# Kernel optimization log

Hardware: AMD Instinct MI355X
Metric: run time of the kernel (lower is better)

The kernel has to match this reference:

```python
import jax, jax.numpy as jnp
import numpy as np

B, T, MEL, C, NL, NSTATE, NFREQ = 16, 1024, 80, 512, 6, 32, 513

def _layer_norm(x, g, b, eps=1e-5):
    mu = x.mean(-1, keepdims=True)
    var = ((x - mu) ** 2).mean(-1, keepdims=True)
    return (x - mu) * jax.lax.rsqrt(var + eps) * g + b

def _s4d(h, logA, Cp, Dp):
    # h: [B,T,C]; diagonal S4D: K[c,t] = sum_n Cp[c,n] * exp(-exp(logA[c,n]) * t)
    t = jnp.arange(T, dtype=h.dtype)
    A = -jnp.exp(logA)                                   # [C,N]
    expA = jnp.exp(A[:, :, None] * t)                    # [C,N,T] Vandermonde
    K = jnp.einsum('cn,cnt->tc', Cp, expA)               # [T,C]
    n_fft = 2 * T
    Xf = jnp.fft.rfft(h, n=n_fft, axis=1)                # [B,F,C]
    Kf = jnp.fft.rfft(K, n=n_fft, axis=0)                # [F,C]
    y = jnp.fft.irfft(Xf * Kf[None], n=n_fft, axis=1)[:, :T, :]
    return jax.nn.gelu(y + Dp * h)

def setup_inputs() -> dict:
    key = jax.random.key(0)
    ks = jax.random.split(key, 16)
    f32 = jnp.float32
    inp = {
        'mel': jax.random.normal(ks[0], (B, T, MEL), f32),
        'w_in': jax.random.normal(ks[1], (MEL, C), f32) * (MEL ** -0.5),
        'b_in': jnp.zeros((C,), f32),
        'freq_emb': jax.random.normal(ks[2], (NFREQ, C), f32) * 0.02,
        's4_logA': jnp.log(0.5 * jnp.ones((NL, C, NSTATE), f32))
                   + 0.1 * jax.random.normal(ks[3], (NL, C, NSTATE), f32),
        's4_C': jax.random.normal(ks[4], (NL, C, NSTATE), f32) * (NSTATE ** -0.5),
        's4_D': jax.random.normal(ks[5], (NL, 1, 1, C), f32),
        'ln_g': jnp.ones((6, C), f32),
        'ln_b': jnp.zeros((6, C), f32),
        'w5': jax.random.normal(ks[6], (5, C), f32) * (C ** -0.5),
        'b5': jnp.zeros((5,), f32),
        'wm': jax.random.normal(ks[7], (C, 13), f32) * (C ** -0.5),
        'bm': jnp.zeros((13,), f32),
    }
    return inp

def reference(mel, w_in, b_in, freq_emb, s4_logA, s4_C, s4_D, ln_g, ln_b, w5, b5, wm, bm):
    x = mel @ w_in + b_in                                # [B,T,C]
    # pad/truncate freq positional embedding along time to T
    if NFREQ >= T:
        freq = freq_emb[:T]
    else:
        pad = jnp.broadcast_to(freq_emb[-1:], (T - NFREQ, C))
        freq = jnp.concatenate([freq_emb, pad], axis=0)
    h = x + freq[None]                                   # [B,T,C]
    for l in range(NL):
        h = _s4d(h, s4_logA[l], s4_C[l], s4_D[l])
    hm = h.mean(axis=1)                                  # [B,C]
    f0        = (_layer_norm(h,  ln_g[0], ln_b[0]) @ w5[0] + b5[0])        # [B,T]
    energy    = (_layer_norm(h,  ln_g[1], ln_b[1]) @ w5[1] + b5[1])        # [B,T]
    pitch_var = (_layer_norm(h,  ln_g[2], ln_b[2]) @ w5[2] + b5[2])        # [B,T]
    speech_rate = (_layer_norm(hm, ln_g[3], ln_b[3]) @ w5[3] + b5[3])[:, None]  # [B,1]
    pause_dur   = (_layer_norm(hm, ln_g[4], ln_b[4]) @ w5[4] + b5[4])[:, None]  # [B,1]
    mfcc        = _layer_norm(hm, ln_g[5], ln_b[5]) @ wm + bm              # [B,13]
    return (f0, energy, pitch_var, speech_rate, pause_dur, mfcc)
```

## Files before the change

kernel.cpp:

```cpp
#include <hip/hip_runtime.h>
#include <hip/hip_bf16.h>

#define B_ 16
#define T_ 1024
#define MEL_ 80
#define C_ 512
#define NL_ 6
#define NS_ 32
#define HBSTR 1096

typedef _Float16 f16x8 __attribute__((ext_vector_type(8)));
typedef float f32x4 __attribute__((ext_vector_type(4)));

__device__ __forceinline__ float wred(float v) {
#pragma unroll
    for (int m = 32; m >= 1; m >>= 1) v += __shfl_xor(v, m, 64);
    return v;
}

__device__ __forceinline__ unsigned int pkh(float a, float b) {
    typedef __fp16 h2 __attribute__((ext_vector_type(2)));
    h2 r = __builtin_amdgcn_cvt_pkrtz(a, b);
    return __builtin_bit_cast(unsigned int, r);
}
__device__ __forceinline__ float h2f(unsigned short u) {
    return (float)__builtin_bit_cast(_Float16, u);
}

__global__ __launch_bounds__(256) void tap_frags(const float* __restrict__ logA,
                                                 const float* __restrict__ Cp,
                                                 const float* __restrict__ Dp,
                                                 unsigned short* __restrict__ AH,
                                                 unsigned short* __restrict__ AL) {
    __shared__ float KT[4][32];
    const int gid0 = blockIdx.x * 4;
    const int tid = threadIdx.x;
    if (tid < 128) {
        int gl = tid >> 5, tau = tid & 31;
        int gid = gid0 + gl;
        const float* la = logA + (size_t)gid * NS_;
        const float* cp = Cp + (size_t)gid * NS_;
        float s = 0.f;
        float t = (float)tau;
#pragma unroll 8
        for (int n = 0; n < NS_; ++n)
            s += cp[n] * expf(-expf(la[n]) * t);
        if (tau == 0) s += Dp[gid];
        KT[gl][tau] = s;
    }
    __syncthreads();
    const int wv = tid >> 6, lane = tid & 63;
    const int gid = gid0 + wv;
    float kv = KT[wv][lane & 31];
    const int m = lane & 15, hh = lane >> 4;
    f16x8 vh, vl;
#pragma unroll
    for (int e = 0; e < 8; ++e) {
        int th = 32 + m - 8 * hh - e;
        int tl = m - 8 * hh - e;
        float a = __shfl(kv, th & 31, 64);
        float bq = __shfl(kv, tl & 31, 64);
        vh[e] = (th >= 0 && th < 32) ? (_Float16)a : (_Float16)0.f;
        vl[e] = (tl >= 0 && tl < 32) ? (_Float16)bq : (_Float16)0.f;
    }
    *(f16x8*)(AH + (size_t)gid * 512 + lane * 8) = vh;
    *(f16x8*)(AL + (size_t)gid * 512 + lane * 8) = vl;
}

__global__ __launch_bounds__(512) void conv_stack(const float* __restrict__ mel,
                                                  const float* __restrict__ w_in,
                                                  const float* __restrict__ b_in,
                                                  const float* __restrict__ freq,
                                                  const unsigned short* __restrict__ AH,
                                                  const unsigned short* __restrict__ AL,
                                                  unsigned short* __restrict__ hfin,
                                                  float* __restrict__ hm) {
    __shared__ unsigned short HB[8 * HBSTR];
    const int b = blockIdx.y;
    const int gx = blockIdx.x;
    const int c0 = 8 * (((gx & 7) << 3) | (gx >> 3));
    const int tid = threadIdx.x;
    const int lane = tid & 63;
    const int wv = tid >> 6;
    const int c = __builtin_amdgcn_readfirstlane(c0 + wv);
    unsigned short* hb = &HB[wv * HBSTR];
    const int n = lane & 15, hh = lane >> 4;

    if (lane < 32) hb[lane] = 0;
    if (lane < 40) hb[1056 + lane] = 0;

    {
        f16x8 Wf[3];
#pragma unroll
        for (int ch = 0; ch < 3; ++ch) {
            f16x8 w;
#pragma unroll
            for (int e = 0; e < 8; ++e) {
                int k = 32 * ch + 8 * hh + e;
                float v = (n < 8 && k < MEL_) ? w_in[(size_t)k * C_ + c0 + n] : 0.f;
                w[e] = (_Float16)v;
            }
            Wf[ch] = w;
        }
        float biasn = (n < 8) ? b_in[c0 + n] : 0.f;
        const float* melb = mel + (size_t)b * T_ * MEL_;
#pragma unroll
        for (int tt = 0; tt < 8; ++tt) {
            const int tbase = 128 * wv + 16 * tt;
            f16x8 Am[3];
#pragma unroll
            for (int ch = 0; ch < 3; ++ch) {
                f16x8 a = {0, 0, 0, 0, 0, 0, 0, 0};
                if (ch < 2 || hh < 2) {
                    const float* mp = melb + (size_t)(tbase + n) * MEL_ + 32 * ch + 8 * hh;
                    float4 m0 = *(const float4*)(mp);
                    float4 m1 = *(const float4*)(mp + 4);
                    a[0] = (_Float16)m0.x; a[1] = (_Float16)m0.y;
                    a[2] = (_Float16)m0.z; a[3] = (_Float16)m0.w;
                    a[4] = (_Float16)m1.x; a[5] = (_Float16)m1.y;
                    a[6] = (_Float16)m1.z; a[7] = (_Float16)m1.w;
                }
                Am[ch] = a;
            }
            f32x4 d = {0.f, 0.f, 0.f, 0.f};
            d = __builtin_amdgcn_mfma_f32_16x16x32_f16(Am[0], Wf[0], d, 0, 0, 0);
            d = __builtin_amdgcn_mfma_f32_16x16x32_f16(Am[1], Wf[1], d, 0, 0, 0);
            d = __builtin_amdgcn_mfma_f32_16x16x32_f16(Am[2], Wf[2], d, 0, 0, 0);
            if (n < 8) {
                float v[4];
#pragma unroll
                for (int r = 0; r < 4; ++r) {
                    int t = tbase + 4 * hh + r;
                    int fr = t < 513 ? t : 512;
                    v[r] = d[r] + biasn + freq[(size_t)fr * C_ + c0 + n];
                }
                uint2 pw;
                pw.x = pkh(v[0], v[1]);
                pw.y = pkh(v[2], v[3]);
                *(uint2*)(&HB[n * HBSTR + 32 + tbase + 4 * hh]) = pw;
            }
        }
    }
    __syncthreads();

    const int boff = 16 * n + 8 * hh;
    const int woff = 32 + 16 * n + 4 * hh;

    f16x8 Ah = *(const f16x8*)(AH + (size_t)c * 512 + lane * 8);
    f16x8 Al = *(const f16x8*)(AL + (size_t)c * 512 + lane * 8);

    float hsum = 0.f;
    for (int l = 0; l < NL_; ++l) {
        const int ln = (l + 1 < NL_) ? l + 1 : 0;
        f16x8 nAh = *(const f16x8*)(AH + ((size_t)ln * C_ + c) * 512 + lane * 8);
        f16x8 nAl = *(const f16x8*)(AL + ((size_t)ln * C_ + c) * 512 + lane * 8);

        f32x4 d[4];
#pragma unroll
        for (int q = 0; q < 4; ++q) {
            const unsigned short* base = hb + 256 * q + boff;
            f16x8 Bh = *(const f16x8*)(base);
            f16x8 Bl = *(const f16x8*)(base + 32);
            f32x4 z = {0.f, 0.f, 0.f, 0.f};
            d[q] = __builtin_amdgcn_mfma_f32_16x16x32_f16(Ah, Bh, z, 0, 0, 0);
            d[q] = __builtin_amdgcn_mfma_f32_16x16x32_f16(Al, Bl, d[q], 0, 0, 0);
        }
#pragma unroll
        for (int q = 0; q < 4; ++q) {
            float g[4];
#pragma unroll
            for (int r = 0; r < 4; ++r) {
                float y = d[q][r];
                float u2 = y * (y * y * 0.07135481627f + 1.59576912161f);
                float rr = __builtin_amdgcn_rcpf(__expf(u2) + 1.f);
                g[r] = y - y * rr;
            }
            if (l == NL_ - 1) hsum += g[0] + g[1] + g[2] + g[3];
            uint2 pw;
            pw.x = pkh(g[0], g[1]);
            pw.y = pkh(g[2], g[3]);
            *(uint2*)(&hb[woff + 256 * q]) = pw;
        }
        Ah = nAh; Al = nAl;
    }

    {
        float s = wred(hsum);
        if (lane == 0) hm[(size_t)b * C_ + c] = s * (1.f / T_);
    }

    __syncthreads();
    {
        unsigned short* dst = hfin + (size_t)b * T_ * C_ + c0;
#pragma unroll
        for (int it = 0; it < 4; ++it) {
            int idx = it * 512 + tid;
            int t = idx >> 1, u = idx & 1;
            unsigned int w0 = (unsigned int)HB[(4 * u + 0) * HBSTR + 32 + t] |
                              ((unsigned int)HB[(4 * u + 1) * HBSTR + 32 + t] << 16);
            unsigned int w1 = (unsigned int)HB[(4 * u + 2) * HBSTR + 32 + t] |
                              ((unsigned int)HB[(4 * u + 3) * HBSTR + 32 + t] << 16);
            uint2 pw = {w0, w1};
            *(uint2*)(dst + (size_t)t * C_ + 4 * u) = pw;
        }
    }
}

__global__ __launch_bounds__(256) void heads_rows(const unsigned short* __restrict__ h,
                                                  const float* __restrict__ ln_g,
                                                  const float* __restrict__ ln_b,
                                                  const float* __restrict__ w5,
                                                  const float* __restrict__ b5,
                                                  float* __restrict__ out) {
    int wv = threadIdx.x >> 6, lane = threadIdx.x & 63;
    int r0 = blockIdx.x * 16 + wv * 4;
    float g[3][8], bb[3][8], ww[3][8];
#pragma unroll
    for (int o = 0; o < 3; ++o) {
        const float* gp = ln_g + o * C_ + lane * 8;
        const float* bp = ln_b + o * C_ + lane * 8;
        const float* wp = w5 + o * C_ + lane * 8;
        float4 a, bq;
        a = *(const float4*)(gp); bq = *(const float4*)(gp + 4);
        g[o][0]=a.x; g[o][1]=a.y; g[o][2]=a.z; g[o][3]=a.w;
        g[o][4]=bq.x; g[o][5]=bq.y; g[o][6]=bq.z; g[o][7]=bq.w;
        a = *(const float4*)(bp); bq = *(const float4*)(bp + 4);
        bb[o][0]=a.x; bb[o][1]=a.y; bb[o][2]=a.z; bb[o][3]=a.w;
        bb[o][4]=bq.x; bb[o][5]=bq.y; bb[o][6]=bq.z; bb[o][7]=bq.w;
        a = *(const float4*)(wp); bq = *(const float4*)(wp + 4);
        ww[o][0]=a.x; ww[o][1]=a.y; ww[o][2]=a.z; ww[o][3]=a.w;
        ww[o][4]=bq.x; ww[o][5]=bq.y; ww[o][6]=bq.z; ww[o][7]=bq.w;
    }
    float b5r[3] = {b5[0], b5[1], b5[2]};
#pragma unroll
    for (int rr = 0; rr < 4; ++rr) {
        const int r = r0 + rr;
        const unsigned short* row = h + (size_t)r * C_ + lane * 8;
        float x[8];
        {
            uint4 q = *(const uint4*)(row);
            x[0] = h2f((unsigned short)(q.x & 0xffff));
            x[1] = h2f((unsigned short)(q.x >> 16));
            x[2] = h2f((unsigned short)(q.y & 0xffff));
            x[3] = h2f((unsigned short)(q.y >> 16));
            x[4] = h2f((unsigned short)(q.z & 0xffff));
            x[5] = h2f((unsigned short)(q.z >> 16));
            x[6] = h2f((unsigned short)(q.w & 0xffff));
            x[7] = h2f((unsigned short)(q.w >> 16));
        }
        float s = 0.f;
#pragma unroll
        for (int i = 0; i < 8; ++i) s += x[i];
        float mu = wred(s) * (1.f / C_);
        float v = 0.f;
#pragma unroll
        for (int i = 0; i < 8; ++i) { float d = x[i] - mu; v += d * d; }
        float rstd = rsqrtf(wred(v) * (1.f / C_) + 1e-5f);
#pragma unroll
        for (int o = 0; o < 3; ++o) {
            float acc = 0.f;
#pragma unroll
            for (int i = 0; i < 8; ++i) {
                float xn = (x[i] - mu) * rstd * g[o][i] + bb[o][i];
                acc += xn * ww[o][i];
            }
            acc = wred(acc);
            if (lane == 0) out[o * (B_ * T_) + r] = acc + b5r[o];
        }
    }
}

__global__ __launch_bounds__(64) void heads_utt(const float* __restrict__ hm,
                                                const float* __restrict__ ln_g,
                                                const float* __restrict__ ln_b,
                                                const float* __restrict__ w5,
                                                const float* __restrict__ b5,
                                                const float* __restrict__ wm,
                                                const float* __restrict__ bm,
                                                float* __restrict__ out) {
    int b = blockIdx.x;
    int lane = threadIdx.x;
    const float* row = hm + (size_t)b * C_;
    float x[8];
#pragma unroll
    for (int i = 0; i < 8; ++i) x[i] = row[lane + 64 * i];
    float s = 0.f;
#pragma unroll
    for (int i = 0; i < 8; ++i) s += x[i];
    float mu = wred(s) * (1.f / C_);
    float v = 0.f;
#pragma unroll
    for (int i = 0; i < 8; ++i) { float d = x[i] - mu; v += d * d; }
    float rstd = rsqrtf(wred(v) * (1.f / C_) + 1e-5f);

    const int OUT_SR = 3 * B_ * T_;
    const int OUT_PD = OUT_SR + B_;
    const int OUT_MF = OUT_PD + B_;
#pragma unroll
    for (int o = 3; o <= 4; ++o) {
        float acc = 0.f;
#pragma unroll
        for (int i = 0; i < 8; ++i) {
            int cc = lane + 64 * i;
            float xn = (x[i] - mu) * rstd * ln_g[o * C_ + cc] + ln_b[o * C_ + cc];
            acc += xn * w5[o * C_ + cc];
        }
        acc = wred(acc);
        if (lane == 0) out[(o == 3 ? OUT_SR : OUT_PD) + b] = acc + b5[o];
    }
    float mf[13];
#pragma unroll
    for (int j = 0; j < 13; ++j) mf[j] = 0.f;
#pragma unroll
    for (int i = 0; i < 8; ++i) {
        int cc = lane + 64 * i;
        float xn = (x[i] - mu) * rstd * ln_g[5 * C_ + cc] + ln_b[5 * C_ + cc];
#pragma unroll
        for (int j = 0; j < 13; ++j) mf[j] += xn * wm[cc * 13 + j];
    }
#pragma unroll
    for (int j = 0; j < 13; ++j) {
        float m = wred(mf[j]);
        if (lane == 0) out[OUT_MF + b * 13 + j] = m + bm[j];
    }
}

extern "C" void kernel_launch(void* const* d_in, const int* in_sizes, int n_in,
                              void* d_out, int out_size, void* d_ws, size_t ws_size,
                              hipStream_t stream) {
    const float* mel   = (const float*)d_in[0];
    const float* w_in  = (const float*)d_in[1];
    const float* b_in  = (const float*)d_in[2];
    const float* freq  = (const float*)d_in[3];
    const float* logA  = (const float*)d_in[4];
    const float* s4C   = (const float*)d_in[5];
    const float* s4D   = (const float*)d_in[6];
    const float* ln_g  = (const float*)d_in[7];
    const float* ln_b  = (const float*)d_in[8];
    const float* w5    = (const float*)d_in[9];
    const float* b5    = (const float*)d_in[10];
    const float* wm    = (const float*)d_in[11];
    const float* bm    = (const float*)d_in[12];
    float* out = (float*)d_out;

    char* ws = (char*)d_ws;
    const size_t H16 = (size_t)B_ * T_ * C_ * sizeof(unsigned short);
    unsigned short* hB16 = (unsigned short*)ws;
    float* hm = (float*)(ws + H16);
    unsigned short* AH = (unsigned short*)(ws + H16 +
                                           (size_t)B_ * C_ * sizeof(float));
    unsigned short* AL = AH + (size_t)NL_ * C_ * 512;

    tap_frags<<<(NL_ * C_) / 4, 256, 0, stream>>>(logA, s4C, s4D, AH, AL);
    conv_stack<<<dim3(C_ / 8, B_), 512, 0, stream>>>(mel, w_in, b_in, freq,
                                                     AH, AL, hB16, hm);
    heads_rows<<<(B_ * T_) / 16, 256, 0, stream>>>(hB16, ln_g, ln_b, w5, b5, out);
    heads_utt<<<B_, 64, 0, stream>>>(hm, ln_g, ln_b, w5, b5, wm, bm, out);
}
```

Measured before the change: 153.4 us.

## Split input projection into separate kernel and store activations in fp32

Moves the mel-to-channel projection and frequency embedding add out of conv_stack into a new in_proj kernel. in_proj writes a channel-major fp32 buffer, and conv_stack loads it into shared memory instead of running MFMA on mel. The final hidden state is now written and read as fp32 instead of fp16, which doubles its traffic to heads_rows. The change adds an extra kernel launch and a full-size fp32 round trip through global memory, apparently in exchange for better precision or simpler staging.

Measured after the change: 154.0 us. No clear change (+0.3%).

```diff
diff --git a/kernel.cpp b/kernel.cpp
--- a/kernel.cpp
+++ b/kernel.cpp
@@ -67,13 +67,71 @@
     *(f16x8*)(AL + (size_t)gid * 512 + lane * 8) = vl;
 }
 
-__global__ __launch_bounds__(512) void conv_stack(const float* __restrict__ mel,
-                                                  const float* __restrict__ w_in,
-                                                  const float* __restrict__ b_in,
-                                                  const float* __restrict__ freq,
+__global__ __launch_bounds__(256) void in_proj(const float* __restrict__ mel,
+                                               const float* __restrict__ w_in,
+                                               const float* __restrict__ b_in,
+                                               const float* __restrict__ freq,
+                                               float* __restrict__ h0T) {
+    const int wid = blockIdx.x * 4 + (threadIdx.x >> 6);
+    const int lane = threadIdx.x & 63;
+    const int mtile = wid >> 1;
+    const int chalf = wid & 1;
+    const int rbase = mtile * 16;
+    const int b = rbase >> 10;
+    const int tloc = rbase & 1023;
+    const int n = lane & 15, hh = lane >> 4;
+
+    f16x8 Am[3];
+#pragma unroll
+    for (int ch = 0; ch < 3; ++ch) {
+        f16x8 a = {0, 0, 0, 0, 0, 0, 0, 0};
+        if (ch < 2 || hh < 2) {
+            const float* mp = mel + (size_t)(rbase + n) * MEL_ + 32 * ch + 8 * hh;
+            float4 m0 = *(const float4*)(mp);
+            float4 m1 = *(const float4*)(mp + 4);
+            a[0] = (_Float16)m0.x; a[1] = (_Float16)m0.y;
+            a[2] = (_Float16)m0.z; a[3] = (_Float16)m0.w;
+            a[4] = (_Float16)m1.x; a[5] = (_Float16)m1.y;
+            a[6] = (_Float16)m1.z; a[7] = (_Float16)m1.w;
+        }
+        Am[ch] = a;
+    }
+
+#pragma unroll 4
+    for (int it = 0; it < 16; ++it) {
+        const int ct = chalf * 256 + it * 16;
+        const int c = ct + n;
+        f16x8 Bw[3];
+#pragma unroll
+        for (int ch = 0; ch < 3; ++ch) {
+            f16x8 w = {0, 0, 0, 0, 0, 0, 0, 0};
+            if (ch < 2 || hh < 2) {
+#pragma unroll
+                for (int e = 0; e < 8; ++e)
+                    w[e] = (_Float16)w_in[(size_t)(32 * ch + 8 * hh + e) * C_ + c];
+            }
+            Bw[ch] = w;
+        }
+        f32x4 d = {0.f, 0.f, 0.f, 0.f};
+        d = __builtin_amdgcn_mfma_f32_16x16x32_f16(Am[0], Bw[0], d, 0, 0, 0);
+        d = __builtin_amdgcn_mfma_f32_16x16x32_f16(Am[1], Bw[1], d, 0, 0, 0);
+        d = __builtin_amdgcn_mfma_f32_16x16x32_f16(Am[2], Bw[2], d, 0, 0, 0);
+        float bias = b_in[c];
+        float4 v;
+#pragma unroll
+        for (int r = 0; r < 4; ++r) {
+            int t = tloc + 4 * hh + r;
+            int fr = t < 513 ? t : 512;
+            ((float*)&v)[r] = d[r] + bias + freq[(size_t)fr * C_ + c];
+        }
+        *(float4*)(h0T + ((size_t)b * C_ + c) * T_ + tloc + 4 * hh) = v;
+    }
+}
+
+__global__ __launch_bounds__(512) void conv_stack(const float* __restrict__ h0T,
+                                                  float* __restrict__ hfin,
                                                   const unsigned short* __restrict__ AH,
                                                   const unsigned short* __restrict__ AL,
-                                                  unsigned short* __restrict__ hfin,
                                                   float* __restrict__ hm) {
     __shared__ unsigned short HB[8 * HBSTR];
     const int b = blockIdx.y;
@@ -84,65 +142,26 @@
     const int wv = tid >> 6;
     const int c = __builtin_amdgcn_readfirstlane(c0 + wv);
     unsigned short* hb = &HB[wv * HBSTR];
-    const int n = lane & 15, hh = lane >> 4;
 
     if (lane < 32) hb[lane] = 0;
     if (lane < 40) hb[1056 + lane] = 0;
 
     {
-        f16x8 Wf[3];
-#pragma unroll
-        for (int ch = 0; ch < 3; ++ch) {
-            f16x8 w;
-#pragma unroll
-            for (int e = 0; e < 8; ++e) {
-                int k = 32 * ch + 8 * hh + e;
-                float v = (n < 8 && k < MEL_) ? w_in[(size_t)k * C_ + c0 + n] : 0.f;
-                w[e] = (_Float16)v;
-            }
-            Wf[ch] = w;
-        }
-        float biasn = (n < 8) ? b_in[c0 + n] : 0.f;
-        const float* melb = mel + (size_t)b * T_ * MEL_;
-#pragma unroll
-        for (int tt = 0; tt < 8; ++tt) {
-            const int tbase = 128 * wv + 16 * tt;
-            f16x8 Am[3];
-#pragma unroll
-            for (int ch = 0; ch < 3; ++ch) {
-                f16x8 a = {0, 0, 0, 0, 0, 0, 0, 0};
-                if (ch < 2 || hh < 2) {
-                    const float* mp = melb + (size_t)(tbase + n) * MEL_ + 32 * ch + 8 * hh;
-                    float4 m0 = *(const float4*)(mp);
-                    float4 m1 = *(const float4*)(mp + 4);
-                    a[0] = (_Float16)m0.x; a[1] = (_Float16)m0.y;
-                    a[2] = (_Float16)m0.z; a[3] = (_Float16)m0.w;
-                    a[4] = (_Float16)m1.x; a[5] = (_Float16)m1.y;
-                    a[6] = (_Float16)m1.z; a[7] = (_Float16)m1.w;
-                }
-                Am[ch] = a;
-            }
-            f32x4 d = {0.f, 0.f, 0.f, 0.f};
-            d = __builtin_amdgcn_mfma_f32_16x16x32_f16(Am[0], Wf[0], d, 0, 0, 0);
-            d = __builtin_amdgcn_mfma_f32_16x16x32_f16(Am[1], Wf[1], d, 0, 0, 0);
-            d = __builtin_amdgcn_mfma_f32_16x16x32_f16(Am[2], Wf[2], d, 0, 0, 0);
-            if (n < 8) {
-                float v[4];
-#pragma unroll
-                for (int r = 0; r < 4; ++r) {
-                    int t = tbase + 4 * hh + r;
-                    int fr = t < 513 ? t : 512;
-                    v[r] = d[r] + biasn + freq[(size_t)fr * C_ + c0 + n];
-                }
-                uint2 pw;
-                pw.x = pkh(v[0], v[1]);
-                pw.y = pkh(v[2], v[3]);
-                *(uint2*)(&HB[n * HBSTR + 32 + tbase + 4 * hh]) = pw;
-            }
-        }
-    }
-    __syncthreads();
-
+        const float* srcT = h0T + ((size_t)b * C_ + c) * T_ + 16 * lane;
+        float4 e0 = *(const float4*)(srcT);
+        float4 e1 = *(const float4*)(srcT + 4);
+        float4 e2 = *(const float4*)(srcT + 8);
+        float4 e3 = *(const float4*)(srcT + 12);
+        uint4 p0, p1;
+        p0.x = pkh(e0.x, e0.y); p0.y = pkh(e0.z, e0.w);
+        p0.z = pkh(e1.x, e1.y); p0.w = pkh(e1.z, e1.w);
+        p1.x = pkh(e2.x, e2.y); p1.y = pkh(e2.z, e2.w);
+        p1.z = pkh(e3.x, e3.y); p1.w = pkh(e3.z, e3.w);
+        *(uint4*)(&hb[32 + 16 * lane]) = p0;
+        *(uint4*)(&hb[32 + 16 * lane + 8]) = p1;
+    }
+
+    const int n = lane & 15, hh = lane >> 4;
     const int boff = 16 * n + 8 * hh;
     const int woff = 32 + 16 * n + 4 * hh;
 
@@ -191,22 +210,22 @@
 
     __syncthreads();
     {
-        unsigned short* dst = hfin + (size_t)b * T_ * C_ + c0;
+        float* dst = hfin + (size_t)b * T_ * C_ + c0;
 #pragma unroll
         for (int it = 0; it < 4; ++it) {
             int idx = it * 512 + tid;
             int t = idx >> 1, u = idx & 1;
-            unsigned int w0 = (unsigned int)HB[(4 * u + 0) * HBSTR + 32 + t] |
-                              ((unsigned int)HB[(4 * u + 1) * HBSTR + 32 + t] << 16);
-            unsigned int w1 = (unsigned int)HB[(4 * u + 2) * HBSTR + 32 + t] |
-                              ((unsigned int)HB[(4 * u + 3) * HBSTR + 32 + t] << 16);
-            uint2 pw = {w0, w1};
-            *(uint2*)(dst + (size_t)t * C_ + 4 * u) = pw;
-        }
-    }
-}
-
-__global__ __launch_bounds__(256) void heads_rows(const unsigned short* __restrict__ h,
+            float4 v;
+            v.x = h2f(HB[(4 * u + 0) * HBSTR + 32 + t]);
+            v.y = h2f(HB[(4 * u + 1) * HBSTR + 32 + t]);
+            v.z = h2f(HB[(4 * u + 2) * HBSTR + 32 + t]);
+            v.w = h2f(HB[(4 * u + 3) * HBSTR + 32 + t]);
+            *(float4*)(dst + (size_t)t * C_ + 4 * u) = v;
+        }
+    }
+}
+
+__global__ __launch_bounds__(256) void heads_rows(const float* __restrict__ h,
                                                   const float* __restrict__ ln_g,
                                                   const float* __restrict__ ln_b,
                                                   const float* __restrict__ w5,
@@ -235,18 +254,13 @@
 #pragma unroll
     for (int rr = 0; rr < 4; ++rr) {
         const int r = r0 + rr;
-        const unsigned short* row = h + (size_t)r * C_ + lane * 8;
+        const float* row = h + (size_t)r * C_ + lane * 8;
         float x[8];
         {
-            uint4 q = *(const uint4*)(row);
-            x[0] = h2f((unsigned short)(q.x & 0xffff));
-            x[1] = h2f((unsigned short)(q.x >> 16));
-            x[2] = h2f((unsigned short)(q.y & 0xffff));
-            x[3] = h2f((unsigned short)(q.y >> 16));
-            x[4] = h2f((unsigned short)(q.z & 0xffff));
-            x[5] = h2f((unsigned short)(q.z >> 16));
-            x[6] = h2f((unsigned short)(q.w & 0xffff));
-            x[7] = h2f((unsigned short)(q.w >> 16));
+            float4 xa = *(const float4*)(row);
+            float4 xb = *(const float4*)(row + 4);
+            x[0]=xa.x; x[1]=xa.y; x[2]=xa.z; x[3]=xa.w;
+            x[4]=xb.x; x[5]=xb.y; x[6]=xb.z; x[7]=xb.w;
         }
         float s = 0.f;
 #pragma unroll
@@ -344,16 +358,17 @@
     float* out = (float*)d_out;
 
     char* ws = (char*)d_ws;
-    const size_t H16 = (size_t)B_ * T_ * C_ * sizeof(unsigned short);
-    unsigned short* hB16 = (unsigned short*)ws;
-    float* hm = (float*)(ws + H16);
-    unsigned short* AH = (unsigned short*)(ws + H16 +
+    const size_t HBYTES = (size_t)B_ * T_ * C_ * sizeof(float);
+    float* hA = (float*)ws;
+    float* hB = (float*)(ws + HBYTES);
+    float* hm = (float*)(ws + 2 * HBYTES);
+    unsigned short* AH = (unsigned short*)(ws + 2 * HBYTES +
                                            (size_t)B_ * C_ * sizeof(float));
     unsigned short* AL = AH + (size_t)NL_ * C_ * 512;
 
     tap_frags<<<(NL_ * C_) / 4, 256, 0, stream>>>(logA, s4C, s4D, AH, AL);
-    conv_stack<<<dim3(C_ / 8, B_), 512, 0, stream>>>(mel, w_in, b_in, freq,
-                                                     AH, AL, hB16, hm);
-    heads_rows<<<(B_ * T_) / 16, 256, 0, stream>>>(hB16, ln_g, ln_b, w5, b5, out);
+    in_proj<<<512, 256, 0, stream>>>(mel, w_in, b_in, freq, hA);
+    conv_stack<<<dim3(C_ / 8, B_), 512, 0, stream>>>(hA, hB, AH, AL, hm);
+    heads_rows<<<(B_ * T_) / 16, 256, 0, stream>>>(hB, ln_g, ln_b, w5, b5, out);
     heads_utt<<<B_, 64, 0, stream>>>(hm, ln_g, ln_b, w5, b5, wm, bm, out);
 }
```
